# Performance work log

Measured on AMD Instinct MI355X. Metric: run time of the kernel, lower is better.

## Reference

```python
import jax, jax.numpy as jnp
import numpy as np

D_MODEL = 512
N_HEADS = 4
D_Q_COMP = 192
D_KV_COMP = 128
QK_NOPE = 64
D_ROT = 32
V_HEAD = 128
D_EXPERT = 1024
N_EXPERTS = 8
N_SHARED = 2
TOP_K = 2
ROPE_THETA = 10000.0
EPS = 1e-6


def setup_inputs() -> dict:
    key = jax.random.key(0)
    ks = jax.random.split(key, 16)
    s = 0.02
    B, S = 4, 2048
    return {
        "x": jax.random.normal(ks[0], (B, S, D_MODEL), jnp.float32),
        "norm2_w": jnp.ones((D_MODEL,), jnp.float32),
        "W_dq": jax.random.normal(ks[1], (D_MODEL, D_Q_COMP), jnp.float32) * s,
        "q_norm_w": jnp.ones((D_Q_COMP,), jnp.float32),
        "W_uq": jax.random.normal(ks[2], (D_Q_COMP, N_HEADS * (QK_NOPE + D_ROT)), jnp.float32) * s,
        "W_dkv": jax.random.normal(ks[3], (D_MODEL, D_KV_COMP + D_ROT), jnp.float32) * s,
        "kv_norm_w": jnp.ones((D_KV_COMP,), jnp.float32),
        "W_ukv": jax.random.normal(ks[4], (D_KV_COMP, N_HEADS * (QK_NOPE + V_HEAD)), jnp.float32) * s,
        "W_o": jax.random.normal(ks[5], (N_HEADS * V_HEAD, D_MODEL), jnp.float32) * s,
        "W_g": jax.random.normal(ks[6], (D_MODEL, N_EXPERTS), jnp.float32) * s,
        "We1": jax.random.normal(ks[7], (N_EXPERTS, D_MODEL, D_EXPERT), jnp.float32) * s,
        "We2": jax.random.normal(ks[8], (N_EXPERTS, D_EXPERT, D_MODEL), jnp.float32) * s,
        "Ws1": jax.random.normal(ks[9], (N_SHARED, D_MODEL, D_EXPERT), jnp.float32) * s,
        "Ws2": jax.random.normal(ks[10], (N_SHARED, D_EXPERT, D_MODEL), jnp.float32) * s,
    }


def rmsnorm(x, w):
    return x * jax.lax.rsqrt(jnp.mean(x * x, axis=-1, keepdims=True) + EPS) * w


def rope_cos_sin(S):
    inv_freq = 1.0 / (ROPE_THETA ** (jnp.arange(0, D_ROT, 2, dtype=jnp.float32) / D_ROT))
    ang = jnp.arange(S, dtype=jnp.float32)[:, None] * inv_freq[None, :]  # [S, D_ROT/2]
    ang = jnp.concatenate([ang, ang], axis=-1)  # [S, D_ROT]
    return jnp.cos(ang), jnp.sin(ang)


def apply_rope(x, cos, sin):
    # x: [..., S, ..., D_ROT] with cos/sin broadcastable; half-rotation convention
    h = D_ROT // 2
    x1, x2 = x[..., :h], x[..., h:]
    rot = jnp.concatenate([-x2, x1], axis=-1)
    return x * cos + rot * sin


def mla_attn(x, W_dq, q_norm_w, W_uq, W_dkv, kv_norm_w, W_ukv, W_o):
    B, S, _ = x.shape
    cq = rmsnorm(x @ W_dq, q_norm_w)                       # [B,S,Dq]
    q = (cq @ W_uq).reshape(B, S, N_HEADS, QK_NOPE + D_ROT)
    q_nope, q_rope = q[..., :QK_NOPE], q[..., QK_NOPE:]
    ckv_full = x @ W_dkv                                   # [B,S,Dkv+Drot] (kv cache)
    c_kv, k_rope = ckv_full[..., :D_KV_COMP], ckv_full[..., D_KV_COMP:]
    kv = (rmsnorm(c_kv, kv_norm_w) @ W_ukv).reshape(B, S, N_HEADS, QK_NOPE + V_HEAD)
    k_nope, v = kv[..., :QK_NOPE], kv[..., QK_NOPE:]
    cos, sin = rope_cos_sin(S)
    q_rope = apply_rope(q_rope, cos[None, :, None, :], sin[None, :, None, :])
    k_rope = apply_rope(k_rope, cos[None, :, :], sin[None, :, :])          # [B,S,Drot]
    k_rope = jnp.broadcast_to(k_rope[:, :, None, :], (B, S, N_HEADS, D_ROT))
    qf = jnp.concatenate([q_nope, q_rope], axis=-1)
    kf = jnp.concatenate([k_nope, k_rope], axis=-1)
    scale = 1.0 / np.sqrt(QK_NOPE + D_ROT)
    scores = jnp.einsum("bqhd,bkhd->bhqk", qf, kf) * scale
    causal = jnp.tril(jnp.ones((S, S), bool))
    scores = jnp.where(causal[None, None], scores, jnp.finfo(scores.dtype).min)
    attn = jax.nn.softmax(scores, axis=-1)
    out = jnp.einsum("bhqk,bkhd->bqhd", attn, v).reshape(B, S, N_HEADS * V_HEAD)
    return out @ W_o, ckv_full


def moe(x, W_g, We1, We2, Ws1, Ws2):
    probs = jax.nn.softmax(x @ W_g, axis=-1)               # [B,S,E]
    top_w, top_i = jax.lax.top_k(probs, TOP_K)
    top_w = top_w / jnp.sum(top_w, axis=-1, keepdims=True)
    one_hot = jax.nn.one_hot(top_i, N_EXPERTS, dtype=x.dtype)   # [B,S,K,E]
    gates = jnp.einsum("bsk,bske->bse", top_w, one_hot)
    h = jax.nn.silu(jnp.einsum("bsd,edh->bseh", x, We1))
    y = jnp.einsum("bseh,ehd->bsed", h, We2)
    routed = jnp.einsum("bsed,bse->bsd", y, gates)
    hs = jax.nn.silu(jnp.einsum("bsd,kdh->bskh", x, Ws1))
    shared = jnp.einsum("bskh,khd->bsd", hs, Ws2)
    mask = jnp.sum(one_hot, axis=2)                        # [B,S,E]
    aux = N_EXPERTS * jnp.sum(jnp.mean(probs, (0, 1)) * jnp.mean(mask, (0, 1))) / TOP_K
    return routed + shared, aux


def reference(x, norm2_w, W_dq, q_norm_w, W_uq, W_dkv, kv_norm_w, W_ukv, W_o, W_g, We1, We2, Ws1, Ws2):
    attn_out, kv = mla_attn(x, W_dq, q_norm_w, W_uq, W_dkv, kv_norm_w, W_ukv, W_o)
    x = x + attn_out
    x = rmsnorm(x, norm2_w)
    moe_out, _ = moe(x, W_g, We1, We2, Ws1, Ws2)
    x = x + moe_out
    return (x, kv)
```

## Files before the change

kernel.cpp:

```cpp
#include <hip/hip_runtime.h>
#include <hip/hip_bf16.h>

typedef __hip_bfloat16 bf16;
typedef __attribute__((ext_vector_type(8))) short short8;
typedef __attribute__((ext_vector_type(8))) __bf16 bf16x8;
typedef __attribute__((ext_vector_type(4))) float f32x4;

#define RT_ROWS 17408
#define SH0_ROW 17408
#define SH1_ROW 25600
#define ROWCAP  33792
#define NTILES  264
#define NCHUNK  288
#define NPART   280

static __device__ __forceinline__ f32x4 mfma16(short8 a, short8 b, f32x4 c) {
  return __builtin_amdgcn_mfma_f32_16x16x32_bf16(
      __builtin_bit_cast(bf16x8, a), __builtin_bit_cast(bf16x8, b), c, 0, 0, 0);
}

static __device__ __forceinline__ void gload16(const bf16* g, void* l) {
  __builtin_amdgcn_global_load_lds(
      (const __attribute__((address_space(1))) void*)g,
      (__attribute__((address_space(3))) void*)l, 16, 0, 0);
}

static __device__ __forceinline__ float b2f(short s) {
  unsigned u = ((unsigned)(unsigned short)s) << 16;
  return __builtin_bit_cast(float, u);
}

__global__ __launch_bounds__(256) void k_f32_to_bf16(const float* __restrict__ in,
                                                     bf16* __restrict__ out, int n) {
  int i = blockIdx.x * 256 + threadIdx.x;
  if (i < n) out[i] = __float2bfloat16(in[i]);
}

struct TD { const float* src; bf16* dst; int K, N, ldo, bx, bxy, start; long inZ, outZ; };
struct Tall { TD d[9]; };

__global__ __launch_bounds__(256) void k_transpose_all(Tall T) {
  int gid = blockIdx.x;
  int si = 0;
  #pragma unroll
  for (int i = 1; i < 9; ++i)
    if (gid >= T.d[i].start) si = i;
  TD dd = T.d[si];
  int local = gid - dd.start;
  int z = local / dd.bxy, rem = local - z * dd.bxy;
  int k0 = (rem % dd.bx) * 64, n0 = (rem / dd.bx) * 64;
  const float* in = dd.src + (size_t)z * dd.inZ;
  bf16* out = dd.dst + (size_t)z * dd.outZ;
  __shared__ bf16 t[64][65];
  for (int rep = 0; rep < 16; ++rep) {
    int lin = rep * 256 + threadIdx.x;
    int i = lin >> 6, j = lin & 63;
    if (k0 + i < dd.K && n0 + j < dd.N)
      t[i][j] = __float2bfloat16(in[(size_t)(k0 + i) * dd.N + n0 + j]);
  }
  __syncthreads();
  for (int rep = 0; rep < 16; ++rep) {
    int lin = rep * 256 + threadIdx.x;
    int jj = lin >> 6, ii = lin & 63;
    if (n0 + jj < dd.N && k0 + ii < dd.K)
      out[(size_t)(n0 + jj) * dd.ldo + k0 + ii] = t[ii][jj];
  }
}

static __device__ __forceinline__ void gemm_core(
    const bf16* __restrict__ A, const bf16* __restrict__ BT,
    int N, int K, int lda, int ldb, int ldc,
    float* __restrict__ Cf, bf16* __restrict__ Cb) {
  __shared__ __align__(16) bf16 As[128 * 32];
  __shared__ __align__(16) bf16 Bs[128 * 32];
  const int m0 = blockIdx.x * 128, n0 = blockIdx.y * 128;
  const int tid = threadIdx.x, lane = tid & 63, wave = tid >> 6;
  const int wr = (wave >> 1) * 64, wc = (wave & 1) * 64;
  const int lr = lane & 15;
  const int kgs = (((lane >> 4) ^ ((lane >> 1) & 3)) << 3);
  const int srow = wave * 16 + (lane >> 2);
  const int scol = (((lane & 3) ^ ((lane >> 3) & 3)) << 3);
  const bf16* Ab = A + (size_t)(m0 + srow) * lda + scol;
  const bf16* Bb = BT + (size_t)(n0 + srow) * ldb + scol;
  char* AsL = (char*)As + wave * 1024;
  char* BsL = (char*)Bs + wave * 1024;

  f32x4 acc[4][4];
  for (int i = 0; i < 4; ++i)
    for (int j = 0; j < 4; ++j) acc[i][j] = f32x4{0.f, 0.f, 0.f, 0.f};

  for (int k0 = 0; k0 < K; k0 += 32) {
    __syncthreads();
    gload16(Ab + k0, AsL);
    gload16(Ab + (size_t)64 * lda + k0, AsL + 4096);
    gload16(Bb + k0, BsL);
    gload16(Bb + (size_t)64 * ldb + k0, BsL + 4096);
    __syncthreads();
    short8 af[4], bfr[4];
    for (int i = 0; i < 4; ++i) af[i] = *(const short8*)&As[(wr + i * 16 + lr) * 32 + kgs];
    for (int j = 0; j < 4; ++j) bfr[j] = *(const short8*)&Bs[(wc + j * 16 + lr) * 32 + kgs];
    for (int i = 0; i < 4; ++i)
      for (int j = 0; j < 4; ++j)
        acc[i][j] = mfma16(af[i], bfr[j], acc[i][j]);
  }

  for (int i = 0; i < 4; ++i) {
    int mb = m0 + wr + i * 16 + (lane >> 4) * 4;
    for (int j = 0; j < 4; ++j) {
      int n = n0 + wc + j * 16 + lr;
      if (n >= N) continue;
      for (int r = 0; r < 4; ++r) {
        size_t idx = (size_t)(mb + r) * ldc + n;
        float v = acc[i][j][r];
        if (Cf) Cf[idx] = v;
        else Cb[idx] = __float2bfloat16(v);
      }
    }
  }
}

__global__ __launch_bounds__(256) void k_gemm_dq(
    const bf16* A, const bf16* BT, int N, int K, int lda, int ldb, int ldc, float* Cf) {
  gemm_core(A, BT, N, K, lda, ldb, ldc, Cf, nullptr);
}
__global__ __launch_bounds__(256) void k_gemm_kv(
    const bf16* A, const bf16* BT, int N, int K, int lda, int ldb, int ldc, bf16* Cb) {
  gemm_core(A, BT, N, K, lda, ldb, ldc, nullptr, Cb);
}
__global__ __launch_bounds__(256) void k_gemm_wo(
    const bf16* A, const bf16* BT, int N, int K, int lda, int ldb, int ldc, bf16* Cb) {
  gemm_core(A, BT, N, K, lda, ldb, ldc, nullptr, Cb);
}

__global__ __launch_bounds__(256) void k_gemm_q(
    const bf16* __restrict__ A, const bf16* __restrict__ BT,
    const float* __restrict__ tab, bf16* __restrict__ qf) {
  const int K = 192, lda = 192, ldb = 192;
  __shared__ __align__(16) bf16 As[128 * 32];
  __shared__ __align__(16) bf16 Bs[128 * 32];
  const int m0 = blockIdx.x * 128, n0 = blockIdx.y * 128;
  const int tid = threadIdx.x, lane = tid & 63, wave = tid >> 6;
  const int wr = (wave >> 1) * 64, wc = (wave & 1) * 64;
  const int lr = lane & 15;
  const int kgs = (((lane >> 4) ^ ((lane >> 1) & 3)) << 3);
  const int srow = wave * 16 + (lane >> 2);
  const int scol = (((lane & 3) ^ ((lane >> 3) & 3)) << 3);
  const bf16* Ab = A + (size_t)(m0 + srow) * lda + scol;
  const bf16* Bb = BT + (size_t)(n0 + srow) * ldb + scol;
  char* AsL = (char*)As + wave * 1024;
  char* BsL = (char*)Bs + wave * 1024;

  f32x4 acc[4][4];
  for (int i = 0; i < 4; ++i)
    for (int j = 0; j < 4; ++j) acc[i][j] = f32x4{0.f, 0.f, 0.f, 0.f};

  for (int k0 = 0; k0 < K; k0 += 32) {
    __syncthreads();
    gload16(Ab + k0, AsL);
    gload16(Ab + (size_t)64 * lda + k0, AsL + 4096);
    gload16(Bb + k0, BsL);
    gload16(Bb + (size_t)64 * ldb + k0, BsL + 4096);
    __syncthreads();
    short8 af[4], bfr[4];
    for (int i = 0; i < 4; ++i) af[i] = *(const short8*)&As[(wr + i * 16 + lr) * 32 + kgs];
    for (int j = 0; j < 4; ++j) bfr[j] = *(const short8*)&Bs[(wc + j * 16 + lr) * 32 + kgs];
    for (int i = 0; i < 4; ++i)
      for (int j = 0; j < 4; ++j)
        acc[i][j] = mfma16(af[i], bfr[j], acc[i][j]);
  }

  #pragma unroll
  for (int i = 0; i < 4; ++i) {
    int mb = m0 + wr + i * 16 + (lane >> 4) * 4;
    #pragma unroll
    for (int j = 0; j < 4; ++j) {
      int n = n0 + wc + j * 16 + lr;
      int h = (n >= 288) ? 3 : ((n >= 192) ? 2 : ((n >= 96) ? 1 : 0));
      int d = n - h * 96;
      #pragma unroll
      for (int r = 0; r < 4; ++r) {
        int t = mb + r;
        int s = t & 2047;
        float v;
        if (d < 64) {
          v = acc[i][j][r];
        } else {
          float c = tab[s * 32 + lr], sn = tab[s * 32 + 16 + lr];
          if (d < 80) {
            float x1 = acc[i][j][r];
            float x2 = (j < 3) ? acc[i][j + 1][r] : 0.f;
            v = x1 * c - x2 * sn;
          } else {
            float x1 = (j > 0) ? acc[i][j - 1][r] : 0.f;
            float x2 = acc[i][j][r];
            v = x2 * c + x1 * sn;
          }
        }
        size_t bh = (size_t)(t >> 11) * 4 + h;
        qf[bh * (2048 * 96) + (size_t)s * 96 + d] = __float2bfloat16(v);
      }
    }
  }
}

template <int ACT>
__global__ __launch_bounds__(256) void k_gemm_grouped(
    const bf16* __restrict__ A, const int* __restrict__ rowtok,
    const int* __restrict__ tileexp, const bf16* __restrict__ W, size_t wstride,
    int N, int K, int lda, bf16* __restrict__ out, int ldo) {
  int bx = (int)blockIdx.x;
  const int tl = (bx & 7) * 33 + (bx >> 3);
  const int ex = tileexp[tl];
  if (ex < 0) return;
  __shared__ __align__(16) bf16 As[128 * 32];
  __shared__ __align__(16) bf16 Bs[128 * 32];
  const int m0 = tl * 128, n0 = blockIdx.y * 128;
  const int tid = threadIdx.x, lane = tid & 63, wave = tid >> 6;
  const int wr = (wave >> 1) * 64, wc = (wave & 1) * 64;
  const int lr = lane & 15;
  const int kgs = (((lane >> 4) ^ ((lane >> 1) & 3)) << 3);
  const int srow = wave * 16 + (lane >> 2);
  const int scol = (((lane & 3) ^ ((lane >> 3) & 3)) << 3);

  int ar0 = m0 + srow, ar1 = ar0 + 64;
  if (rowtok) {
    int t0 = rowtok[ar0]; ar0 = (t0 < 0) ? 0 : t0;
    int t1 = rowtok[ar1]; ar1 = (t1 < 0) ? 0 : t1;
  }
  const bf16* A0 = A + (size_t)ar0 * lda + scol;
  const bf16* A1 = A + (size_t)ar1 * lda + scol;
  const bf16* BT = W + (size_t)ex * wstride;
  const bf16* B0 = BT + (size_t)(n0 + srow) * K + scol;
  const bf16* B1 = B0 + (size_t)64 * K;
  char* AsL = (char*)As + wave * 1024;
  char* BsL = (char*)Bs + wave * 1024;

  f32x4 acc[4][4];
  for (int i = 0; i < 4; ++i)
    for (int j = 0; j < 4; ++j) acc[i][j] = f32x4{0.f, 0.f, 0.f, 0.f};

  for (int k0 = 0; k0 < K; k0 += 32) {
    __syncthreads();
    gload16(A0 + k0, AsL);
    gload16(A1 + k0, AsL + 4096);
    gload16(B0 + k0, BsL);
    gload16(B1 + k0, BsL + 4096);
    __syncthreads();
    short8 af[4], bfr[4];
    for (int i = 0; i < 4; ++i) af[i] = *(const short8*)&As[(wr + i * 16 + lr) * 32 + kgs];
    for (int j = 0; j < 4; ++j) bfr[j] = *(const short8*)&Bs[(wc + j * 16 + lr) * 32 + kgs];
    for (int i = 0; i < 4; ++i)
      for (int j = 0; j < 4; ++j)
        acc[i][j] = mfma16(af[i], bfr[j], acc[i][j]);
  }

  for (int i = 0; i < 4; ++i) {
    int mb = m0 + wr + i * 16 + (lane >> 4) * 4;
    for (int j = 0; j < 4; ++j) {
      int n = n0 + wc + j * 16 + lr;
      for (int r = 0; r < 4; ++r) {
        float v = acc[i][j][r];
        if (ACT) v = v / (1.f + __expf(-v));
        out[(size_t)(mb + r) * ldo + n] = __float2bfloat16(v);
      }
    }
  }
}

__global__ __launch_bounds__(256) void k_postproj1(
    const float* __restrict__ tmp, const float* __restrict__ qnw,
    const float* __restrict__ kvnw, bf16* __restrict__ cq,
    bf16* __restrict__ kvn, float* __restrict__ krope, float* __restrict__ kvout) {
  int t = blockIdx.x * 4 + (threadIdx.x >> 6);
  int lane = threadIdx.x & 63;
  const float* row = tmp + (size_t)t * 352;
  float s1 = 0.f, s2 = 0.f;
  for (int d = lane; d < 192; d += 64) { float v = row[d]; s1 += v * v; }
  for (int d = lane; d < 128; d += 64) { float v = row[192 + d]; s2 += v * v; }
  for (int o = 32; o > 0; o >>= 1) { s1 += __shfl_xor(s1, o); s2 += __shfl_xor(s2, o); }
  float r1 = rsqrtf(s1 / 192.f + 1e-6f);
  float r2 = rsqrtf(s2 / 128.f + 1e-6f);
  for (int d = lane; d < 192; d += 64)
    cq[(size_t)t * 192 + d] = __float2bfloat16(row[d] * r1 * qnw[d]);
  for (int d = lane; d < 128; d += 64)
    kvn[(size_t)t * 128 + d] = __float2bfloat16(row[192 + d] * r2 * kvnw[d]);
  for (int d = lane; d < 160; d += 64)
    kvout[(size_t)t * 160 + d] = row[192 + d];
  if (lane < 32) krope[(size_t)t * 32 + lane] = row[320 + lane];
}

__global__ __launch_bounds__(256) void k_rope_table(float* __restrict__ tab) {
  int idx = blockIdx.x * 256 + threadIdx.x;
  int s = idx >> 4, jm = idx & 15;
  float invf = expf(-(float)jm * 0.575646273f);
  float ang = (float)s * invf;
  tab[s * 32 + jm] = cosf(ang);
  tab[s * 32 + 16 + jm] = sinf(ang);
}

__global__ __launch_bounds__(256) void k_make_kf(const bf16* __restrict__ kvbig,
                                                 const float* __restrict__ krope,
                                                 const float* __restrict__ tab,
                                                 bf16* __restrict__ kf) {
  int idx = blockIdx.x * 256 + threadIdx.x;
  int t = idx / 384, hd = idx - t * 384;
  int h = hd / 96, d = hd - h * 96;
  int s = t & 2047;
  bf16 outv;
  if (d < 64) outv = kvbig[(size_t)t * 768 + h * 192 + d];
  else {
    int j = d - 64, jm = j & 15;
    float c = tab[s * 32 + jm], sn = tab[s * 32 + 16 + jm];
    float x1 = krope[(size_t)t * 32 + jm], x2 = krope[(size_t)t * 32 + 16 + jm];
    float v = (j < 16) ? (x1 * c - x2 * sn) : (x2 * c + x1 * sn);
    outv = __float2bfloat16(v);
  }
  size_t bh = (size_t)(t >> 11) * 4 + h;
  kf[bh * (2048 * 96) + (size_t)s * 96 + d] = outv;
}

__global__ __launch_bounds__(256) void k_make_vT(const bf16* __restrict__ kvbig,
                                                 bf16* __restrict__ vT) {
  __shared__ bf16 t[64][136];
  int bh = blockIdx.y;
  int b = bh >> 2, h = bh & 3;
  int s0 = blockIdx.x * 64;
  for (int rep = 0; rep < 4; ++rep) {
    int lin = rep * 256 + threadIdx.x;
    int i = lin >> 4, jc = (lin & 15) * 8;
    short8 v = *(const short8*)(kvbig + (size_t)(b * 2048 + s0 + i) * 768 + h * 192 + 64 + jc);
    *(short8*)&t[i][jc] = v;
  }
  __syncthreads();
  for (int rep = 0; rep < 32; ++rep) {
    int lin = rep * 256 + threadIdx.x;
    int d = lin >> 6, i = lin & 63;
    vT[((size_t)bh * 128 + d) * 2048 + s0 + i] = t[i][d];
  }
}

__global__ __launch_bounds__(64, 2) void k_flash(const bf16* __restrict__ qf,
                                                 const bf16* __restrict__ kf,
                                                 const bf16* __restrict__ vT,
                                                 bf16* __restrict__ attn,
                                                 bf16* __restrict__ pO,
                                                 float* __restrict__ pML) {
  const int lin = (int)blockIdx.x;
  const int r16 = lin & 15;
  const int bh = ((r16 & 7) << 1) | (r16 >> 3);
  const int e = (NCHUNK - 1) - (lin >> 4);
  int k = 0;
  #pragma unroll
  for (int kk = 1; kk < 8; ++kk)
    if (e >= 4 * kk * (kk + 1)) k = kk;
  const int rel = e - 4 * k * (k + 1);
  const int Q = 8 * k + rel / (k + 1);
  const int c = rel - (rel / (k + 1)) * (k + 1);
  const int nt = (Q >> 1) + 1;
  const int kt0 = 4 * c;
  const int kt1 = (kt0 + 4 < nt) ? kt0 + 4 : nt;
  const int q0 = Q * 32;
  const int lane = threadIdx.x;
  const int lr = lane & 15, hi = lane >> 4, kg = hi * 8;
  const bf16* Qp = qf + (size_t)bh * (2048 * 96);
  const bf16* Kp = kf + (size_t)bh * (2048 * 96);
  const bf16* Vt = vT + (size_t)bh * (128 * 2048);

  short8 qfr[2][3];
  for (int i = 0; i < 2; ++i)
    for (int ks = 0; ks < 3; ++ks)
      qfr[i][ks] = *(const short8*)(Qp + (size_t)(q0 + i * 16 + lr) * 96 + ks * 32 + kg);

  f32x4 o[2][8];
  for (int i = 0; i < 2; ++i)
    for (int j = 0; j < 8; ++j) o[i][j] = f32x4{0.f, 0.f, 0.f, 0.f};
  float mrow[2][4], lsum[2][4];
  for (int i = 0; i < 2; ++i)
    for (int r = 0; r < 4; ++r) { mrow[i][r] = -1e30f; lsum[i][r] = 0.f; }

  __shared__ bf16 plds[32][72];
  const float scale = 0.1020620726f;

  for (int kt = kt0; kt < kt1; ++kt) {
    int kv0 = kt * 64;
    f32x4 s[2][4];
    for (int i = 0; i < 2; ++i)
      for (int j = 0; j < 4; ++j) s[i][j] = f32x4{0.f, 0.f, 0.f, 0.f};
    for (int jh = 0; jh < 2; ++jh) {
      short8 kc[2][3];
      for (int jj = 0; jj < 2; ++jj)
        for (int ks = 0; ks < 3; ++ks)
          kc[jj][ks] = *(const short8*)(Kp + (size_t)(kv0 + (jh * 2 + jj) * 16 + lr) * 96 + ks * 32 + kg);
      for (int jj = 0; jj < 2; ++jj)
        for (int ks = 0; ks < 3; ++ks) {
          s[0][jh * 2 + jj] = mfma16(qfr[0][ks], kc[jj][ks], s[0][jh * 2 + jj]);
          s[1][jh * 2 + jj] = mfma16(qfr[1][ks], kc[jj][ks], s[1][jh * 2 + jj]);
        }
    }

    bool diag = (kt == nt - 1);
    for (int i = 0; i < 2; ++i)
      for (int j = 0; j < 4; ++j)
        for (int r = 0; r < 4; ++r) {
          float v = s[i][j][r] * scale;
          if (diag) {
            int qq = q0 + i * 16 + hi * 4 + r;
            int kk = kv0 + j * 16 + lr;
            if (kk > qq) v = -1e30f;
          }
          s[i][j][r] = v;
        }
    float vmax4[2][4], grow = -1e30f;
    for (int i = 0; i < 2; ++i)
      for (int r = 0; r < 4; ++r) {
        float v = fmaxf(fmaxf(s[i][0][r], s[i][1][r]), fmaxf(s[i][2][r], s[i][3][r]));
        v = fmaxf(v, __shfl_xor(v, 1));
        v = fmaxf(v, __shfl_xor(v, 2));
        v = fmaxf(v, __shfl_xor(v, 4));
        v = fmaxf(v, __shfl_xor(v, 8));
        vmax4[i][r] = v;
        grow = fmaxf(grow, v - mrow[i][r]);
      }
    if (!__all(grow <= 8.f)) {
      for (int i = 0; i < 2; ++i)
        for (int r = 0; r < 4; ++r) {
          float mnew = fmaxf(mrow[i][r], vmax4[i][r]);
          float alpha = __expf(mrow[i][r] - mnew);
          mrow[i][r] = mnew;
          lsum[i][r] *= alpha;
          for (int j = 0; j < 8; ++j) o[i][j][r] *= alpha;
        }
    }
    for (int i = 0; i < 2; ++i)
      for (int r = 0; r < 4; ++r) {
        float rs = 0.f;
        for (int j = 0; j < 4; ++j) {
          float p = __expf(s[i][j][r] - mrow[i][r]);
          s[i][j][r] = p;
          rs += p;
        }
        rs += __shfl_xor(rs, 1); rs += __shfl_xor(rs, 2);
        rs += __shfl_xor(rs, 4); rs += __shfl_xor(rs, 8);
        lsum[i][r] += rs;
      }
    for (int i = 0; i < 2; ++i)
      for (int j = 0; j < 4; ++j)
        for (int r = 0; r < 4; ++r)
          plds[i * 16 + hi * 4 + r][j * 16 + lr] = __float2bfloat16(s[i][j][r]);
    short8 pf[2][2];
    for (int i = 0; i < 2; ++i) {
      pf[i][0] = *(const short8*)&plds[i * 16 + lr][kg];
      pf[i][1] = *(const short8*)&plds[i * 16 + lr][32 + kg];
    }
    for (int j = 0; j < 8; ++j) {
      short8 v0 = *(const short8*)(Vt + (size_t)(j * 16 + lr) * 2048 + kv0 + kg);
      short8 v1 = *(const short8*)(Vt + (size_t)(j * 16 + lr) * 2048 + kv0 + 32 + kg);
      o[0][j] = mfma16(pf[0][0], v0, o[0][j]);
      o[0][j] = mfma16(pf[0][1], v1, o[0][j]);
      o[1][j] = mfma16(pf[1][0], v0, o[1][j]);
      o[1][j] = mfma16(pf[1][1], v1, o[1][j]);
    }
  }

  if (k == 0) {
    int bb = bh >> 2, h = bh & 3;
    for (int i = 0; i < 2; ++i)
      for (int r = 0; r < 4; ++r) {
        int qq = q0 + i * 16 + hi * 4 + r;
        float inv = 1.f / lsum[i][r];
        size_t baseo = ((size_t)(bb * 2048 + qq)) * 512 + h * 128;
        for (int j = 0; j < 8; ++j)
          attn[baseo + j * 16 + lr] = __float2bfloat16(o[i][j][r] * inv);
      }
  } else {
    const int p = bh * NPART + (e - 8);
    for (int i = 0; i < 2; ++i)
      for (int r = 0; r < 4; ++r) {
        int qrl = i * 16 + hi * 4 + r;
        size_t baseo = (size_t)p * 4096 + (size_t)qrl * 128;
        for (int j = 0; j < 8; ++j)
          pO[baseo + j * 16 + lr] = __float2bfloat16(o[i][j][r]);
        if (lr == 0) {
          pML[p * 64 + qrl] = mrow[i][r];
          pML[p * 64 + 32 + qrl] = lsum[i][r];
        }
      }
  }
}

__global__ __launch_bounds__(512) void k_merge(const bf16* __restrict__ pO,
                                               const float* __restrict__ pML,
                                               bf16* __restrict__ attn) {
  const int Q = 8 + blockIdx.x;
  const int bh = blockIdx.y;
  const int k = Q >> 3, np = k + 1;
  const int eb = 4 * k * (k + 1) + (Q - 8 * k) * (k + 1);
  const int pbase = bh * NPART + (eb - 8);
  const int qrl = threadIdx.x >> 4, d0 = (threadIdx.x & 15) * 8;
  float m[8], l[8], w[8];
  float mm = -1e30f;
  for (int i = 0; i < 8; ++i)
    if (i < np) {
      m[i] = pML[(pbase + i) * 64 + qrl];
      l[i] = pML[(pbase + i) * 64 + 32 + qrl];
      mm = fmaxf(mm, m[i]);
    }
  float L = 0.f;
  for (int i = 0; i < 8; ++i)
    if (i < np) { w[i] = __expf(m[i] - mm); L += l[i] * w[i]; }
  float inv = 1.f / L;
  float acc[8];
  for (int u = 0; u < 8; ++u) acc[u] = 0.f;
  for (int i = 0; i < 8; ++i)
    if (i < np) {
      short8 v = *(const short8*)(pO + (size_t)(pbase + i) * 4096 + (size_t)qrl * 128 + d0);
      for (int u = 0; u < 8; ++u) acc[u] += b2f(v[u]) * w[i];
    }
  int bb = bh >> 2, h = bh & 3;
  int q = Q * 32 + qrl;
  size_t ob = ((size_t)(bb * 2048 + q)) * 512 + h * 128 + d0;
  for (int u = 0; u < 8; ++u)
    attn[ob + u] = __float2bfloat16(acc[u] * inv);
}

__global__ __launch_bounds__(256) void k_norm2g(const float* __restrict__ x,
                                                const bf16* __restrict__ wo,
                                                const float* __restrict__ w,
                                                const float* __restrict__ Wg,
                                                float* __restrict__ x2f,
                                                bf16* __restrict__ x2b,
                                                int* __restrict__ tokexp,
                                                float* __restrict__ tokgate) {
  int wv = threadIdx.x >> 6, lane = threadIdx.x & 63;
  int t = blockIdx.x * 4 + wv;
  const float* row = x + (size_t)t * 512;
  int d0 = lane * 8;
  float v[8];
  {
    float4 a = *(const float4*)(row + d0);
    float4 bb = *(const float4*)(row + d0 + 4);
    short8 wv8 = *(const short8*)(wo + (size_t)t * 512 + d0);
    v[0] = a.x + b2f(wv8[0]); v[1] = a.y + b2f(wv8[1]);
    v[2] = a.z + b2f(wv8[2]); v[3] = a.w + b2f(wv8[3]);
    v[4] = bb.x + b2f(wv8[4]); v[5] = bb.y + b2f(wv8[5]);
    v[6] = bb.z + b2f(wv8[6]); v[7] = bb.w + b2f(wv8[7]);
  }
  float ss = 0.f;
  for (int u = 0; u < 8; ++u) ss += v[u] * v[u];
  for (int o = 32; o > 0; o >>= 1) ss += __shfl_xor(ss, o);
  float rr = rsqrtf(ss / 512.f + 1e-6f);
  {
    float4 a = *(const float4*)(w + d0);
    float4 bb = *(const float4*)(w + d0 + 4);
    v[0] *= rr * a.x; v[1] *= rr * a.y; v[2] *= rr * a.z; v[3] *= rr * a.w;
    v[4] *= rr * bb.x; v[5] *= rr * bb.y; v[6] *= rr * bb.z; v[7] *= rr * bb.w;
  }
  float* xo = x2f + (size_t)t * 512 + d0;
  bf16* xb = x2b + (size_t)t * 512 + d0;
  for (int u = 0; u < 8; ++u) { xo[u] = v[u]; xb[u] = __float2bfloat16(v[u]); }
  float p[8];
  for (int ee = 0; ee < 8; ++ee) p[ee] = 0.f;
  for (int u = 0; u < 8; ++u) {
    float4 g0 = *(const float4*)(Wg + (size_t)(d0 + u) * 8);
    float4 g1 = *(const float4*)(Wg + (size_t)(d0 + u) * 8 + 4);
    p[0] += v[u] * g0.x; p[1] += v[u] * g0.y; p[2] += v[u] * g0.z; p[3] += v[u] * g0.w;
    p[4] += v[u] * g1.x; p[5] += v[u] * g1.y; p[6] += v[u] * g1.z; p[7] += v[u] * g1.w;
  }
  for (int o = 32; o > 0; o >>= 1)
    for (int ee = 0; ee < 8; ++ee) p[ee] += __shfl_xor(p[ee], o);
  if (lane == 0) {
    float mx = -1e30f;
    for (int ee = 0; ee < 8; ++ee) mx = fmaxf(mx, p[ee]);
    for (int ee = 0; ee < 8; ++ee) p[ee] = __expf(p[ee] - mx);
    int i1 = 0; float v1 = p[0];
    for (int ee = 1; ee < 8; ++ee) if (p[ee] > v1) { v1 = p[ee]; i1 = ee; }
    int i2 = -1; float v2 = -1.f;
    for (int ee = 0; ee < 8; ++ee) if (ee != i1 && p[ee] > v2) { v2 = p[ee]; i2 = ee; }
    float ws = v1 + v2;
    tokexp[t * 2] = i1; tokexp[t * 2 + 1] = i2;
    tokgate[t * 2] = v1 / ws; tokgate[t * 2 + 1] = v2 / ws;
  }
}

__global__ __launch_bounds__(256) void k_count(const int* __restrict__ tokexp,
                                               int* __restrict__ counts) {
  __shared__ int lc[8];
  if (threadIdx.x < 8) lc[threadIdx.x] = 0;
  __syncthreads();
  int i = blockIdx.x * 256 + threadIdx.x;
  atomicAdd(&lc[tokexp[i]], 1);
  __syncthreads();
  if (threadIdx.x < 8) atomicAdd(&counts[threadIdx.x], lc[threadIdx.x]);
}

__global__ __launch_bounds__(256) void k_moe_setup(const int* __restrict__ counts,
                                                   int* __restrict__ segstart,
                                                   int* __restrict__ tileexp,
                                                   int* __restrict__ rowtok) {
  __shared__ int ss[9], cc[8];
  if (threadIdx.x < 8) cc[threadIdx.x] = counts[threadIdx.x];
  __syncthreads();
  if (threadIdx.x == 0) {
    int off = 0;
    for (int e = 0; e < 8; ++e) { ss[e] = off; off += ((cc[e] + 127) >> 7) << 7; }
    ss[8] = off;
    for (int e = 0; e < 9; ++e) segstart[e] = ss[e];
  }
  __syncthreads();
  for (int tl = threadIdx.x; tl < NTILES; tl += 256) {
    int ex;
    if (tl >= 200) ex = 9;
    else if (tl >= 136) ex = 8;
    else {
      int row = tl * 128; ex = -1;
      for (int i = 0; i < 8; ++i)
        if (row >= ss[i] && row < ss[i + 1]) { ex = i; break; }
    }
    tileexp[tl] = ex;
  }
  for (int e = 0; e < 8; ++e) {
    int cnt = cc[e], cap = ((cnt + 127) >> 7) << 7;
    for (int r = cnt + threadIdx.x; r < cap; r += 256)
      rowtok[ss[e] + r] = -1;
  }
}

__global__ __launch_bounds__(256) void k_assign(const int* __restrict__ tokexp,
                                                int* __restrict__ fill,
                                                const int* __restrict__ segstart,
                                                int* __restrict__ rowtok,
                                                int* __restrict__ tokslot) {
  __shared__ int lcnt[8], lbase[8];
  if (threadIdx.x < 8) lcnt[threadIdx.x] = 0;
  __syncthreads();
  int t = blockIdx.x * 256 + threadIdx.x;
  int e0 = tokexp[t * 2], e1 = tokexp[t * 2 + 1];
  int r0 = atomicAdd(&lcnt[e0], 1);
  int r1 = atomicAdd(&lcnt[e1], 1);
  __syncthreads();
  if (threadIdx.x < 8) lbase[threadIdx.x] = atomicAdd(&fill[threadIdx.x], lcnt[threadIdx.x]);
  __syncthreads();
  int p0 = segstart[e0] + lbase[e0] + r0;
  int p1 = segstart[e1] + lbase[e1] + r1;
  rowtok[p0] = t; rowtok[p1] = t;
  tokslot[t * 2] = p0; tokslot[t * 2 + 1] = p1;
  rowtok[SH0_ROW + t] = t;
  rowtok[SH1_ROW + t] = t;
}

__global__ __launch_bounds__(256) void k_combine(const float* __restrict__ x2f,
                                                 const bf16* __restrict__ Yg,
                                                 const int* __restrict__ tokslot,
                                                 const float* __restrict__ tokgate,
                                                 float* __restrict__ out_x) {
  int t = blockIdx.x * 4 + (threadIdx.x >> 6);
  int lane = threadIdx.x & 63;
  int s1 = tokslot[t * 2], s2 = tokslot[t * 2 + 1];
  float g1 = tokgate[t * 2], g2 = tokgate[t * 2 + 1];
  int d0 = lane * 8;
  short8 a = *(const short8*)(Yg + (size_t)s1 * 512 + d0);
  short8 b = *(const short8*)(Yg + (size_t)s2 * 512 + d0);
  short8 c = *(const short8*)(Yg + (size_t)(SH0_ROW + t) * 512 + d0);
  short8 d = *(const short8*)(Yg + (size_t)(SH1_ROW + t) * 512 + d0);
  const float* xr = x2f + (size_t)t * 512 + d0;
  float* outr = out_x + (size_t)t * 512 + d0;
  for (int u = 0; u < 8; ++u)
    outr[u] = xr[u] + g1 * b2f(a[u]) + g2 * b2f(b[u]) + b2f(c[u]) + b2f(d[u]);
}

extern "C" void kernel_launch(void* const* d_in, const int* in_sizes, int n_in,
                              void* d_out, int out_size, void* d_ws, size_t ws_size,
                              hipStream_t stream) {
  const float* x    = (const float*)d_in[0];
  const float* n2w  = (const float*)d_in[1];
  const float* Wdq  = (const float*)d_in[2];
  const float* qnw  = (const float*)d_in[3];
  const float* Wuq  = (const float*)d_in[4];
  const float* Wdkv = (const float*)d_in[5];
  const float* kvnw = (const float*)d_in[6];
  const float* Wukv = (const float*)d_in[7];
  const float* Wo   = (const float*)d_in[8];
  const float* Wg   = (const float*)d_in[9];
  const float* We1  = (const float*)d_in[10];
  const float* We2  = (const float*)d_in[11];
  const float* Ws1  = (const float*)d_in[12];
  const float* Ws2  = (const float*)d_in[13];

  float* out_x  = (float*)d_out;
  float* out_kv = out_x + (size_t)4 * 2048 * 512;

  char* base = (char*)d_ws;
  size_t off = 0;
  auto alloc = [&](size_t bytes) -> void* {
    void* p = base + off;
    off += (bytes + 255) & ~(size_t)255;
    return p;
  };
  const size_t T = 8192;
  bf16*  WcatT = (bf16*)alloc(352 * 512 * 2);
  bf16*  WuqT  = (bf16*)alloc(384 * 192 * 2);
  bf16*  WukvT = (bf16*)alloc(768 * 128 * 2);
  bf16*  WoT   = (bf16*)alloc(512 * 512 * 2);
  bf16*  W1T   = (bf16*)alloc((size_t)10 * 1024 * 512 * 2);
  bf16*  W2T   = (bf16*)alloc((size_t)10 * 512 * 1024 * 2);
  float* x2f   = (float*)alloc(T * 512 * 4);
  bf16*  x2b   = (bf16*)alloc(T * 512 * 2);
  int*   tokexp  = (int*)alloc(T * 2 * 4);
  float* tokgate = (float*)alloc(T * 2 * 4);
  int*   tokslot = (int*)alloc(T * 2 * 4);
  int*   rowtok  = (int*)alloc(ROWCAP * 4);
  int*   segstart= (int*)alloc(16 * 4);
  int*   tileexp = (int*)alloc(NTILES * 4);
  int*   cnts    = (int*)alloc(16 * 4);
  float* ropet   = (float*)alloc(2048 * 32 * 4);

  char* S = base + off;
  size_t soff = 0;
  auto salloc = [&](size_t bytes) -> void* {
    void* p = S + soff;
    soff += (bytes + 255) & ~(size_t)255;
    return p;
  };
  bf16*  xb    = (bf16*)salloc(T * 512 * 2);
  float* tmp0  = (float*)salloc(T * 352 * 4);
  bf16*  cq    = (bf16*)salloc(T * 192 * 2);
  bf16*  kvn   = (bf16*)salloc(T * 128 * 2);
  float* krope = (float*)salloc(T * 32 * 4);
  bf16*  kvbig = (bf16*)salloc(T * 768 * 2);
  bf16*  qf    = (bf16*)salloc(T * 384 * 2);
  bf16*  kf    = (bf16*)salloc(T * 384 * 2);
  bf16*  vT    = (bf16*)salloc(T * 512 * 2);
  bf16*  attnb = (bf16*)salloc(T * 512 * 2);
  bf16*  woout = (bf16*)salloc(T * 512 * 2);
  bf16*  pO    = (bf16*)salloc((size_t)16 * NPART * 4096 * 2);
  float* pML   = (float*)salloc((size_t)16 * NPART * 64 * 4);
  size_t attn_ws = soff;
  bf16* Hg = (bf16*)S;
  bf16* Yg = (bf16*)(S + (size_t)ROWCAP * 1024 * 2 + 256);
  size_t moe_ws = (size_t)ROWCAP * 1024 * 2 + 256 + (size_t)ROWCAP * 512 * 2;
  size_t need = off + (attn_ws > moe_ws ? attn_ws : moe_ws);
  if (need > ws_size) return;

  hipMemsetAsync(cnts, 0, 64, stream);

  k_f32_to_bf16<<<(int)((T * 512 + 255) / 256), 256, 0, stream>>>(x, xb, (int)(T * 512));
  k_rope_table<<<128, 256, 0, stream>>>(ropet);

  {
    Tall TT;
    auto mk = [](const float* s, bf16* d, int K, int N, int ldo, int nz,
                 long inZ, long outZ, int start) -> TD {
      TD t; t.src = s; t.dst = d; t.K = K; t.N = N; t.ldo = ldo;
      t.bx = (K + 63) / 64; t.bxy = t.bx * ((N + 63) / 64);
      t.start = start; t.inZ = inZ; t.outZ = outZ; (void)nz; return t;
    };
    int st = 0;
    TT.d[0] = mk(Wdq,  WcatT,             512, 192, 512, 1, 0, 0, st); st += 24;
    TT.d[1] = mk(Wdkv, WcatT + 192 * 512, 512, 160, 512, 1, 0, 0, st); st += 24;
    TT.d[2] = mk(Wuq,  WuqT,  192, 384, 192, 1, 0, 0, st); st += 18;
    TT.d[3] = mk(Wukv, WukvT, 128, 768, 128, 1, 0, 0, st); st += 24;
    TT.d[4] = mk(Wo,   WoT,   512, 512, 512, 1, 0, 0, st); st += 64;
    TT.d[5] = mk(We1, W1T, 512, 1024, 512, 8, (long)512 * 1024, (long)1024 * 512, st); st += 1024;
    TT.d[6] = mk(Ws1, W1T + (size_t)8 * 1024 * 512, 512, 1024, 512, 2,
                 (long)512 * 1024, (long)1024 * 512, st); st += 256;
    TT.d[7] = mk(We2, W2T, 1024, 512, 1024, 8, (long)1024 * 512, (long)512 * 1024, st); st += 1024;
    TT.d[8] = mk(Ws2, W2T + (size_t)8 * 512 * 1024, 1024, 512, 1024, 2,
                 (long)1024 * 512, (long)512 * 1024, st); st += 256;
    k_transpose_all<<<st, 256, 0, stream>>>(TT);
  }

  k_gemm_dq<<<dim3(64, 3), 256, 0, stream>>>(xb, WcatT, 352, 512, 512, 512, 352, tmp0);
  k_postproj1<<<2048, 256, 0, stream>>>(tmp0, qnw, kvnw, cq, kvn, krope, out_kv);

  k_gemm_q<<<dim3(64, 3), 256, 0, stream>>>(cq, WuqT, ropet, qf);

  k_gemm_kv<<<dim3(64, 6), 256, 0, stream>>>(kvn, WukvT, 768, 128, 128, 128, 768, kvbig);
  k_make_kf<<<12288, 256, 0, stream>>>(kvbig, krope, ropet, kf);
  k_make_vT<<<dim3(32, 16), 256, 0, stream>>>(kvbig, vT);

  k_flash<<<NCHUNK * 16, 64, 0, stream>>>(qf, kf, vT, attnb, pO, pML);
  k_merge<<<dim3(56, 16), 512, 0, stream>>>(pO, pML, attnb);

  k_gemm_wo<<<dim3(64, 4), 256, 0, stream>>>(attnb, WoT, 512, 512, 512, 512, 512, woout);
  k_norm2g<<<2048, 256, 0, stream>>>(x, woout, n2w, Wg, x2f, x2b, tokexp, tokgate);
  k_count<<<64, 256, 0, stream>>>(tokexp, cnts);
  k_moe_setup<<<1, 256, 0, stream>>>(cnts, segstart, tileexp, rowtok);
  k_assign<<<32, 256, 0, stream>>>(tokexp, cnts + 8, segstart, rowtok, tokslot);

  k_gemm_grouped<1><<<dim3(NTILES, 8), 256, 0, stream>>>(
      x2b, rowtok, tileexp, W1T, (size_t)1024 * 512, 1024, 512, 512, Hg, 1024);
  k_gemm_grouped<0><<<dim3(NTILES, 4), 256, 0, stream>>>(
      Hg, nullptr, tileexp, W2T, (size_t)512 * 1024, 512, 1024, 1024, Yg, 512);
  k_combine<<<2048, 256, 0, stream>>>(x2f, Yg, tokslot, tokgate, out_x);
}
```

Measured before the change: 346.4 us.

## Double-buffer LDS tiles in grouped MoE GEMM to overlap loads with MFMA

The grouped expert GEMM now keeps two LDS buffers for the A and B tiles. It issues global-to-LDS loads for the next K slice before computing on the current one, then uses one waitcnt plus barrier per iteration instead of two syncthreads. This is meant to hide global load latency behind MFMA work. It doubles LDS use per block (32 KB), which may reduce occupancy, and the barrier ordering has to stay correct so a buffer is not overwritten while other waves still read it.

```diff
diff --git a/kernel.cpp b/kernel.cpp
--- a/kernel.cpp
+++ b/kernel.cpp
@@ -212,8 +212,8 @@
   const int tl = (bx & 7) * 33 + (bx >> 3);
   const int ex = tileexp[tl];
   if (ex < 0) return;
-  __shared__ __align__(16) bf16 As[128 * 32];
-  __shared__ __align__(16) bf16 Bs[128 * 32];
+  __shared__ __align__(16) bf16 As[2][128 * 32];
+  __shared__ __align__(16) bf16 Bs[2][128 * 32];
   const int m0 = tl * 128, n0 = blockIdx.y * 128;
   const int tid = threadIdx.x, lane = tid & 63, wave = tid >> 6;
   const int wr = (wave >> 1) * 64, wc = (wave & 1) * 64;
@@ -232,24 +232,50 @@
   const bf16* BT = W + (size_t)ex * wstride;
   const bf16* B0 = BT + (size_t)(n0 + srow) * K + scol;
   const bf16* B1 = B0 + (size_t)64 * K;
-  char* AsL = (char*)As + wave * 1024;
-  char* BsL = (char*)Bs + wave * 1024;
-
-  f32x4 acc[4][4];
-  for (int i = 0; i < 4; ++i)
-    for (int j = 0; j < 4; ++j) acc[i][j] = f32x4{0.f, 0.f, 0.f, 0.f};
-
-  for (int k0 = 0; k0 < K; k0 += 32) {
-    __syncthreads();
+
+  auto stage = [&](int buf, int k0) {
+    char* AsL = (char*)As[buf] + wave * 1024;
+    char* BsL = (char*)Bs[buf] + wave * 1024;
     gload16(A0 + k0, AsL);
     gload16(A1 + k0, AsL + 4096);
     gload16(B0 + k0, BsL);
     gload16(B1 + k0, BsL + 4096);
-    __syncthreads();
+  };
+
+  f32x4 acc[4][4];
+  for (int i = 0; i < 4; ++i)
+    for (int j = 0; j < 4; ++j) acc[i][j] = f32x4{0.f, 0.f, 0.f, 0.f};
+
+  stage(0, 0);
+  asm volatile("s_waitcnt vmcnt(0)" ::: "memory");
+  __builtin_amdgcn_s_barrier();
+
+  int cur = 0;
+  for (int k0 = 32; k0 < K; k0 += 32) {
+    stage(cur ^ 1, k0);
     short8 af[4], bfr[4];
-    for (int i = 0; i < 4; ++i) af[i] = *(const short8*)&As[(wr + i * 16 + lr) * 32 + kgs];
-    for (int j = 0; j < 4; ++j) bfr[j] = *(const short8*)&Bs[(wc + j * 16 + lr) * 32 + kgs];
+    #pragma unroll
+    for (int i = 0; i < 4; ++i) af[i] = *(const short8*)&As[cur][(wr + i * 16 + lr) * 32 + kgs];
+    #pragma unroll
+    for (int j = 0; j < 4; ++j) bfr[j] = *(const short8*)&Bs[cur][(wc + j * 16 + lr) * 32 + kgs];
+    #pragma unroll
     for (int i = 0; i < 4; ++i)
+      #pragma unroll
+      for (int j = 0; j < 4; ++j)
+        acc[i][j] = mfma16(af[i], bfr[j], acc[i][j]);
+    asm volatile("s_waitcnt vmcnt(0)" ::: "memory");
+    __builtin_amdgcn_s_barrier();
+    cur ^= 1;
+  }
+  {
+    short8 af[4], bfr[4];
+    #pragma unroll
+    for (int i = 0; i < 4; ++i) af[i] = *(const short8*)&As[cur][(wr + i * 16 + lr) * 32 + kgs];
+    #pragma unroll
+    for (int j = 0; j < 4; ++j) bfr[j] = *(const short8*)&Bs[cur][(wc + j * 16 + lr) * 32 + kgs];
+    #pragma unroll
+    for (int i = 0; i < 4; ++i)
+      #pragma unroll
       for (int j = 0; j < 4; ++j)
         acc[i][j] = mfma16(af[i], bfr[j], acc[i][j]);
   }
```

New measurement: 352.1 us. About the same (+1.7%).
